# Performance work log

Measured on AMD Instinct MI355X. Metric: run time of the kernel, lower is better.

Reference implementation:

```python
import math
import jax, jax.numpy as jnp
import numpy as np

B, L, CIN, COUT = 128, 100, 55, 55
D, H, DFF, MODES = 512, 8, 512, 32
E = D // H
KERNELS = (12, 24)
NK = len(KERNELS)


def _pos_emb(length, d):
    pos = np.arange(length)[:, None].astype(np.float32)
    div = np.exp(np.arange(0, d, 2).astype(np.float32) * (-math.log(10000.0) / d))
    pe = np.zeros((length, d), dtype=np.float32)
    pe[:, 0::2] = np.sin(pos * div)
    pe[:, 1::2] = np.cos(pos * div)
    return jnp.asarray(pe)


def _circ_conv3(x, W):
    # Conv1d(kernel=3, padding=1, padding_mode='circular', bias=False); x:(B,L,C) W:(O,C,3)
    n = x.shape[1]
    xp = jnp.concatenate([x[:, -1:], x, x[:, :1]], axis=1)
    return (jnp.einsum('blc,oc->blo', xp[:, 0:n], W[:, :, 0]) +
            jnp.einsum('blc,oc->blo', xp[:, 1:n + 1], W[:, :, 1]) +
            jnp.einsum('blc,oc->blo', xp[:, 2:n + 2], W[:, :, 2]))


def _moving_avg(x, k):
    # replicate-pad then length-preserving mean filter (Autoformer moving_avg)
    front = jnp.repeat(x[:, :1], (k - 1) // 2, axis=1)
    end = jnp.repeat(x[:, -1:], k // 2, axis=1)
    xp = jnp.concatenate([front, x, end], axis=1)
    c = jnp.cumsum(xp, axis=1)
    c = jnp.concatenate([jnp.zeros_like(c[:, :1]), c], axis=1)
    return (c[:, k:] - c[:, :-k]) / float(k)


def _decomp(x, w, b):
    # series_decomp_multi with learned softmax mixing (Linear(1, NK))
    means = jnp.stack([_moving_avg(x, k) for k in KERNELS], axis=-1)  # (B,L,D,NK)
    mix = jax.nn.softmax(x[..., None] * w + b, axis=-1)
    mean = jnp.sum(means * mix, axis=-1)
    return x - mean, mean


def _my_layernorm(x, g, b):
    mu = x.mean(-1, keepdims=True)
    var = ((x - mu) ** 2).mean(-1, keepdims=True)
    xh = (x - mu) / jnp.sqrt(var + 1e-5) * g + b
    return xh - xh.mean(axis=1, keepdims=True)


def _fourier_block(q, Wc):
    # q:(B,L,H,E) -> rfft over L, per-mode complex GEMM with Wc:(H,E,E,MODES), irfft
    x = jnp.transpose(q, (0, 2, 3, 1))  # (B,H,E,L)
    xf = jnp.fft.rfft(x, axis=-1)
    sel = jnp.einsum('bhem,heom->bhom', xf[..., :MODES], Wc)
    nfreq = x.shape[-1] // 2 + 1
    out_ft = jnp.zeros(sel.shape[:-1] + (nfreq,), sel.dtype).at[..., :MODES].set(sel)
    out = jnp.fft.irfft(out_ft, n=x.shape[-1], axis=-1)
    return jnp.transpose(out, (0, 3, 1, 2))  # (B,L,H,E)


def _fourier_cross(q, k, Wc):
    # FourierCrossAttention: frequency-domain q*k attention with tanh activation, values = k
    xq = jnp.transpose(q, (0, 2, 3, 1))
    xk = jnp.transpose(k, (0, 2, 3, 1))
    qf = jnp.fft.rfft(xq, axis=-1)[..., :MODES]
    kf = jnp.fft.rfft(xk, axis=-1)[..., :MODES]
    qk = jnp.tanh(jnp.einsum('bhex,bhey->bhxy', qf, kf))
    qkv = jnp.einsum('bhxy,bhey->bhex', qk, kf)
    w = jnp.einsum('bhex,heox->bhox', qkv, Wc)
    nfreq = xq.shape[-1] // 2 + 1
    out_ft = jnp.zeros(w.shape[:-1] + (nfreq,), w.dtype).at[..., :MODES].set(w)
    out = jnp.fft.irfft(out_ft / float(D * D), n=xq.shape[-1], axis=-1)
    return jnp.transpose(out, (0, 3, 1, 2))


def _heads(x, W, b):
    y = x @ W.T + b
    return y.reshape(y.shape[0], y.shape[1], H, E)


def _gelu(x):
    return jax.nn.gelu(x, approximate=False)


def _forward(x, emb_enc_w, emb_dec_w, enc_proj_w, enc_proj_b, enc_sig_w, enc_sig_b,
             enc_four_wr, enc_four_wi, enc_ffn_w1, enc_ffn_w2, enc_dcmp_w, enc_dcmp_b,
             enc_norm_g, enc_norm_b, dec_proj_w, dec_proj_b, dec_four_wr, dec_four_wi,
             crs_proj_w, crs_proj_b, crs_four_wr, crs_four_wi, dec_ffn_w1, dec_ffn_w2,
             dec_dcmp_w, dec_dcmp_b, dec_trend_w, dec_norm_g, dec_norm_b,
             out_proj_w, out_proj_b):
    b, n, _ = x.shape
    dist = jnp.abs(jnp.arange(n)[:, None] - jnp.arange(n)[None, :]).astype(x.dtype)
    # seasonal-trend init decomposition
    trend_init = jnp.broadcast_to(x.mean(axis=1, keepdims=True), x.shape)
    seasonal_init = x - trend_init
    pe = _pos_emb(n, D)
    enc_four = enc_four_wr + 1j * enc_four_wi
    enc = _circ_conv3(x, emb_enc_w) + pe
    series_l, prior_l, sigma_l = [], [], []
    for i in range(enc_proj_w.shape[0]):  # e_layers (structurally distinct params)
        Wp, bp = enc_proj_w[i], enc_proj_b[i]
        q = _heads(enc, Wp[0], bp[0])
        k = _heads(enc, Wp[1], bp[1])
        v = _heads(enc, Wp[2], bp[2])  # projected but unused by FourierBlock (faithful)
        attn_out = _fourier_block(q, enc_four).reshape(b, n, D) @ Wp[3].T + bp[3]
        # Anomaly-Transformer association: series = softmax(QK^T/sqrt(E)), prior = Gaussian kernel
        scores = jnp.einsum('blhe,bshe->bhls', q, k) / math.sqrt(E)
        series = jax.nn.softmax(scores, axis=-1)
        sig = jnp.transpose(enc @ enc_sig_w[i].T + enc_sig_b[i], (0, 2, 1))  # (B,H,L)
        sig = jnp.power(3.0, jax.nn.sigmoid(5.0 * sig) + 1e-5) - 1.0
        prior = jnp.exp(-dist ** 2 / (2.0 * sig[..., None] ** 2)) / (math.sqrt(2.0 * math.pi) * sig[..., None])
        series_l.append(series); prior_l.append(prior); sigma_l.append(sig)
        h = enc + attn_out
        h, _ = _decomp(h, enc_dcmp_w[i, 0], enc_dcmp_b[i, 0])
        y = _gelu(h @ enc_ffn_w1[i].T) @ enc_ffn_w2[i].T
        enc, _ = _decomp(h + y, enc_dcmp_w[i, 1], enc_dcmp_b[i, 1])
    enc = _my_layernorm(enc, enc_norm_g, enc_norm_b)

    # decoder (d_layers = 1)
    dec = _circ_conv3(seasonal_init, emb_dec_w) + pe
    dec_four = dec_four_wr + 1j * dec_four_wi
    crs_four = crs_four_wr + 1j * crs_four_wi
    q = _heads(dec, dec_proj_w[0], dec_proj_b[0])
    sa = _fourier_block(q, dec_four).reshape(b, n, D) @ dec_proj_w[3].T + dec_proj_b[3]
    h = dec + sa
    h, t1 = _decomp(h, dec_dcmp_w[0], dec_dcmp_b[0])
    qc = _heads(h, crs_proj_w[0], crs_proj_b[0])
    kc = _heads(enc, crs_proj_w[1], crs_proj_b[1])
    ca = _fourier_cross(qc, kc, crs_four).reshape(b, n, D) @ crs_proj_w[3].T + crs_proj_b[3]
    h = h + ca
    h, t2 = _decomp(h, dec_dcmp_w[1], dec_dcmp_b[1])
    y = _gelu(h @ dec_ffn_w1.T) @ dec_ffn_w2.T
    h, t3 = _decomp(h + y, dec_dcmp_w[2], dec_dcmp_b[2])
    residual_trend = _circ_conv3(t1 + t2 + t3, dec_trend_w)  # (B,L,COUT)
    trend = trend_init + residual_trend
    h = _my_layernorm(h, dec_norm_g, dec_norm_b)
    seasonal = h @ out_proj_w.T + out_proj_b
    dec_out = trend + seasonal
    return dec_out, jnp.stack(series_l), jnp.stack(prior_l), jnp.stack(sigma_l)


def setup_inputs() -> dict:
    key = jax.random.key(0)
    ks = iter(jax.random.split(key, 64))

    def rn(shape, s=0.02):
        return s * jax.random.normal(next(ks), shape, dtype=jnp.float32)

    return dict(
        x=jax.random.normal(next(ks), (B, L, CIN), dtype=jnp.float32),
        emb_enc_w=rn((D, CIN, 3)), emb_dec_w=rn((D, CIN, 3)),
        enc_proj_w=rn((2, 4, D, D)), enc_proj_b=jnp.zeros((2, 4, D), jnp.float32),
        enc_sig_w=rn((2, H, D)), enc_sig_b=jnp.zeros((2, H), jnp.float32),
        enc_four_wr=rn((H, E, E, MODES)), enc_four_wi=rn((H, E, E, MODES)),
        enc_ffn_w1=rn((2, DFF, D)), enc_ffn_w2=rn((2, D, DFF)),
        enc_dcmp_w=rn((2, 2, NK), 1.0), enc_dcmp_b=jnp.zeros((2, 2, NK), jnp.float32),
        enc_norm_g=jnp.ones((D,), jnp.float32), enc_norm_b=jnp.zeros((D,), jnp.float32),
        dec_proj_w=rn((4, D, D)), dec_proj_b=jnp.zeros((4, D), jnp.float32),
        dec_four_wr=rn((H, E, E, MODES)), dec_four_wi=rn((H, E, E, MODES)),
        crs_proj_w=rn((4, D, D)), crs_proj_b=jnp.zeros((4, D), jnp.float32),
        crs_four_wr=rn((H, E, E, MODES)), crs_four_wi=rn((H, E, E, MODES)),
        dec_ffn_w1=rn((DFF, D)), dec_ffn_w2=rn((D, DFF)),
        dec_dcmp_w=rn((3, NK), 1.0), dec_dcmp_b=jnp.zeros((3, NK), jnp.float32),
        dec_trend_w=rn((COUT, D, 3)),
        dec_norm_g=jnp.ones((D,), jnp.float32), dec_norm_b=jnp.zeros((D,), jnp.float32),
        out_proj_w=rn((COUT, D)), out_proj_b=jnp.zeros((COUT,), jnp.float32),
    )


def reference(x, emb_enc_w, emb_dec_w, enc_proj_w, enc_proj_b, enc_sig_w, enc_sig_b,
              enc_four_wr, enc_four_wi, enc_ffn_w1, enc_ffn_w2, enc_dcmp_w, enc_dcmp_b,
              enc_norm_g, enc_norm_b, dec_proj_w, dec_proj_b, dec_four_wr, dec_four_wi,
              crs_proj_w, crs_proj_b, crs_four_wr, crs_four_wi, dec_ffn_w1, dec_ffn_w2,
              dec_dcmp_w, dec_dcmp_b, dec_trend_w, dec_norm_g, dec_norm_b,
              out_proj_w, out_proj_b):
    return _forward(x, emb_enc_w, emb_dec_w, enc_proj_w, enc_proj_b, enc_sig_w, enc_sig_b,
                    enc_four_wr, enc_four_wi, enc_ffn_w1, enc_ffn_w2, enc_dcmp_w, enc_dcmp_b,
                    enc_norm_g, enc_norm_b, dec_proj_w, dec_proj_b, dec_four_wr, dec_four_wi,
                    crs_proj_w, crs_proj_b, crs_four_wr, crs_four_wi, dec_ffn_w1, dec_ffn_w2,
                    dec_dcmp_w, dec_dcmp_b, dec_trend_w, dec_norm_g, dec_norm_b,
                    out_proj_w, out_proj_b)
```

## Files before the change

### kernel.cpp

```cpp
#include <hip/hip_runtime.h>
#include <hip/hip_bf16.h>
#include <cmath>

constexpr int B = 128, L = 100, CIN = 55, COUT = 55;
constexpr int D = 512, H = 8, DFF = 512, MODES = 32, E = 64;
constexpr int NK = 2;
constexpr int M_ROWS = B * L;
constexpr int KEMB = 192;
constexpr size_t BLD  = (size_t)B * L * D;
constexpr size_t BHEM = (size_t)B * H * E * MODES;
constexpr size_t BHLL = (size_t)B * H * L * L;
constexpr float INV_SQRT_2PI = 0.3989422804014327f;

static inline int cdiv(int a, int b) { return (a + b - 1) / b; }

typedef short shortx8 __attribute__((ext_vector_type(8)));
typedef float f32x4 __attribute__((ext_vector_type(4)));

__device__ inline unsigned short f2bf(float f)
{
    unsigned int u = __float_as_uint(f);
    unsigned int r = (u + 0x7FFFu + ((u >> 16) & 1u)) >> 16;
    return (unsigned short)r;
}
__device__ inline unsigned short f2bf_n(float f)
{
    union { __hip_bfloat16 h; unsigned short u; } cv;
    cv.h = __float2bfloat16(f);
    return cv.u;
}
__device__ inline float bf2f(unsigned short u)
{
    union { unsigned int i; float f; } c;
    c.i = (unsigned int)u << 16;
    return c.f;
}

__global__ void init_consts(float* __restrict__ pe)
{
    int idx = blockIdx.x * 256 + threadIdx.x;
    if (idx < L * D) {
        int l = idx / D, d = idx % D;
        int i2 = d & ~1;
        float div = expf((float)i2 * (-logf(10000.f) / (float)D));
        float ang = (float)l * div;
        pe[idx] = (d & 1) ? cosf(ang) : sinf(ang);
    }
}

__global__ void init_tw(unsigned short* __restrict__ twf, unsigned short* __restrict__ twi)
{
    int idx = blockIdx.x * 256 + threadIdx.x;
    if (idx >= 64 * 128) return;
    {
        int mp = idx / 128, t = idx % 128;
        float v = 0.f;
        if (t < L) {
            if (mp < 32) v = cosf(2.f * 3.14159265358979323846f * (float)mp * (float)t / (float)L);
            else v = -sinf(2.f * 3.14159265358979323846f * (float)(mp - 32) * (float)t / (float)L);
        }
        twf[idx] = f2bf(v);
    }
    {
        int t = idx / 64, mp = idx % 64;
        float v = 0.f;
        if (t < L) {
            if (mp == 0) v = 1.f;
            else if (mp < 32) v = 2.f * cosf(2.f * 3.14159265358979323846f * (float)mp * (float)t / (float)L);
            else if (mp == 32) v = 0.f;
            else v = -2.f * sinf(2.f * 3.14159265358979323846f * (float)(mp - 32) * (float)t / (float)L);
        }
        twi[idx] = f2bf(v);
    }
}

__global__ void xmean_kernel(const float* __restrict__ x, float* __restrict__ xm)
{
    int idx = blockIdx.x * 256 + threadIdx.x;
    if (idx >= B * CIN) return;
    int b = idx / CIN, c = idx % CIN;
    float s = 0.f;
    for (int l = 0; l < L; ++l) s += x[((size_t)b * L + l) * CIN + c];
    xm[idx] = s * (1.f / (float)L);
}

struct PrepArgs {
    const float* src[7];
    unsigned short* dst[7];
    int n4[7];
    const float* emb_enc; const float* emb_dec; const float* trend_w; const float* seas_w;
    unsigned short* d_embenc; unsigned short* d_embdec; unsigned short* d_trd; unsigned short* d_seas;
};
__global__ __launch_bounds__(256) void prep_all(PrepArgs a, int total4, int padTotal)
{
    for (int i = blockIdx.x * 256 + threadIdx.x; i < total4 + padTotal; i += gridDim.x * 256) {
        if (i < total4) {
            int idx = i, s = 0;
            while (idx >= a.n4[s]) { idx -= a.n4[s]; ++s; }
            float4 v = *(const float4*)&a.src[s][(size_t)idx * 4];
            ushort4 h;
            h.x = f2bf(v.x); h.y = f2bf(v.y); h.z = f2bf(v.z); h.w = f2bf(v.w);
            *(ushort4*)&a.dst[s][(size_t)idx * 4] = h;
            continue;
        }
        int p = i - total4;
        if (p < D * KEMB) {
            int r = p / KEMB, k = p % KEMB;
            a.d_embenc[p] = (k < CIN * 3) ? f2bf(a.emb_enc[(size_t)r * (CIN * 3) + k]) : (unsigned short)0;
        } else if ((p -= D * KEMB) < D * KEMB) {
            int r = p / KEMB, k = p % KEMB;
            a.d_embdec[p] = (k < CIN * 3) ? f2bf(a.emb_dec[(size_t)r * (CIN * 3) + k]) : (unsigned short)0;
        } else if ((p -= D * KEMB) < 192 * D) {
            int n = p / D, d = p % D;
            int j = n / 64, o = n % 64;
            a.d_trd[p] = (o < COUT) ? f2bf(a.trend_w[(size_t)o * (D * 3) + d * 3 + j]) : (unsigned short)0;
        } else {
            p -= 192 * D;
            int r = p / D, k = p % D;
            a.d_seas[p] = (r < COUT) ? f2bf(a.seas_w[(size_t)r * D + k]) : (unsigned short)0;
        }
    }
}

__global__ __launch_bounds__(256) void transpose_w(const float* __restrict__ wr, const float* __restrict__ wi,
                                                   float2* __restrict__ wt)
{
    int h = blockIdx.x / E, e = blockIdx.x % E;
    __shared__ float tr[64][33], ti[64][33];
    for (int i = threadIdx.x; i < E * MODES; i += 256) {
        int o = i / MODES, m = i % MODES;
        size_t s = (((size_t)h * E + e) * E + o) * MODES + m;
        tr[o][m] = wr[s]; ti[o][m] = wi[s];
    }
    __syncthreads();
    for (int i = threadIdx.x; i < MODES * E; i += 256) {
        int m = i / E, o = i % E;
        wt[(((size_t)h * MODES + m) * E + e) * E + o] = make_float2(tr[o][m], ti[o][m]);
    }
}

__global__ void im2col_emb(const float* __restrict__ x, const float* __restrict__ xmean,
                           unsigned short* __restrict__ A2)
{
    int idx = blockIdx.x * 256 + threadIdx.x;
    if (idx >= M_ROWS * KEMB) return;
    int k = idx % KEMB, m = idx / KEMB;
    float v = 0.f;
    if (k < CIN * 3) {
        int c = k / 3, j = k % 3;
        int l = m % L, b = m / L;
        int ls = l + j - 1; ls = (ls + L) % L;
        v = x[((size_t)b * L + ls) * CIN + c];
        if (xmean) v -= xmean[(size_t)b * CIN + c];
    }
    A2[idx] = f2bf(v);
}

template<int BN>
__global__ __launch_bounds__(256) void gemm_mfma(const unsigned short* __restrict__ A,
                                                 const unsigned short* __restrict__ Wb,
                                                 const float* __restrict__ bias, const float* __restrict__ pe,
                                                 float* __restrict__ C, unsigned short* __restrict__ Cb,
                                                 int Nout, int K, int act, int accum)
{
    constexpr int NI = BN / 32;
    constexpr int BI = BN / 64;
    __shared__ unsigned short As[2][128][40];
    __shared__ unsigned short Bs[2][BN][40];
    int tid = threadIdx.x;
    int row0 = blockIdx.y * 128, col0 = blockIdx.x * BN;
    int wid = tid >> 6, lane = tid & 63;
    int wm = wid >> 1, wn = wid & 1;
    int lrow = lane & 15, kg = lane >> 4;
    int ar = tid >> 2, ac8 = (tid & 3) * 8;
    f32x4 acc[4][NI] = {};
    shortx8 rah[2], rbh[BI];

    auto loadG = [&](int k0) {
#pragma unroll
        for (int p = 0; p < 2; ++p)
            rah[p] = *(const shortx8*)&A[(size_t)(row0 + p * 64 + ar) * K + k0 + ac8];
#pragma unroll
        for (int p = 0; p < BI; ++p)
            rbh[p] = *(const shortx8*)&Wb[(size_t)(col0 + p * 64 + ar) * K + k0 + ac8];
    };
    auto storeLDS = [&](int buf) {
#pragma unroll
        for (int p = 0; p < 2; ++p)
            *(shortx8*)&As[buf][p * 64 + ar][ac8] = rah[p];
#pragma unroll
        for (int p = 0; p < BI; ++p)
            *(shortx8*)&Bs[buf][p * 64 + ar][ac8] = rbh[p];
    };

    int nk = K >> 5;
    loadG(0);
    storeLDS(0);
    if (nk > 1) loadG(32);
    __syncthreads();
    int cur = 0;
    for (int s = 0; s < nk; ++s) {
        if (s + 1 < nk) {
            storeLDS(cur ^ 1);
            if (s + 2 < nk) loadG((s + 2) << 5);
        }
        shortx8 av[4], bv[NI];
#pragma unroll
        for (int mi = 0; mi < 4; ++mi)
            av[mi] = *(const shortx8*)&As[cur][wm * 64 + mi * 16 + lrow][kg * 8];
#pragma unroll
        for (int ni = 0; ni < NI; ++ni)
            bv[ni] = *(const shortx8*)&Bs[cur][wn * (BN / 2) + ni * 16 + lrow][kg * 8];
#pragma unroll
        for (int mi = 0; mi < 4; ++mi)
#pragma unroll
            for (int ni = 0; ni < NI; ++ni)
                acc[mi][ni] = __builtin_amdgcn_mfma_f32_16x16x32_bf16(av[mi], bv[ni], acc[mi][ni], 0, 0, 0);
        if (s + 1 < nk) __syncthreads();
        cur ^= 1;
    }
#pragma unroll
    for (int mi = 0; mi < 4; ++mi) {
#pragma unroll
        for (int ni = 0; ni < NI; ++ni) {
            int col = col0 + wn * (BN / 2) + ni * 16 + lrow;
            if (col >= Nout) continue;
#pragma unroll
            for (int r = 0; r < 4; ++r) {
                int row = row0 + wm * 64 + mi * 16 + kg * 4 + r;
                float v = acc[mi][ni][r];
                if (bias) v += bias[col];
                if (pe) v += pe[(size_t)(row % L) * Nout + col];
                if (act) v = 0.5f * v * (1.f + erff(v * 0.70710678118654752f));
                size_t o = (size_t)row * Nout + col;
                if (Cb) Cb[o] = f2bf_n(v);
                else if (accum) C[o] += v;
                else C[o] = v;
            }
        }
    }
}

__global__ __launch_bounds__(256) void scores_softmax(const unsigned short* __restrict__ QK,
                                                      float* __restrict__ out)
{
    int bh = blockIdx.x, b = bh / H, h = bh % H;
    int pass = blockIdx.y;
    __shared__ unsigned short Ks[112][72];
    __shared__ unsigned short Qs[64][72];
    int tid = threadIdx.x;
    int srow = tid >> 4, sc4 = (tid & 15) * 4;
#pragma unroll
    for (int i = 0; i < 7; ++i) {
        int r = i * 16 + srow;
        ushort4 hh = {0, 0, 0, 0};
        if (r < L) hh = *(const ushort4*)&QK[((size_t)b * L + r) * 1024 + 512 + h * E + sc4];
        *(ushort4*)&Ks[r][sc4] = hh;
    }
#pragma unroll
    for (int i = 0; i < 4; ++i) {
        int r = i * 16 + srow;
        int gr = pass * 64 + r;
        ushort4 hh = {0, 0, 0, 0};
        if (gr < L) hh = *(const ushort4*)&QK[((size_t)b * L + gr) * 1024 + h * E + sc4];
        *(ushort4*)&Qs[r][sc4] = hh;
    }
    __syncthreads();
    int wid = tid >> 6, lane = tid & 63;
    int lrow = lane & 15, kg = lane >> 4;
    f32x4 acc[7] = {};
#pragma unroll
    for (int ks = 0; ks < 2; ++ks) {
        shortx8 aq = *(const shortx8*)&Qs[wid * 16 + lrow][ks * 32 + kg * 8];
#pragma unroll
        for (int tj = 0; tj < 7; ++tj) {
            shortx8 bk = *(const shortx8*)&Ks[tj * 16 + lrow][ks * 32 + kg * 8];
            acc[tj] = __builtin_amdgcn_mfma_f32_16x16x32_bf16(aq, bk, acc[tj], 0, 0, 0);
        }
    }
    float mx[4] = {-1e30f, -1e30f, -1e30f, -1e30f};
#pragma unroll
    for (int tj = 0; tj < 7; ++tj) {
        bool valid = (tj * 16 + lrow) < L;
#pragma unroll
        for (int r = 0; r < 4; ++r) {
            float v = acc[tj][r] * 0.125f;
            acc[tj][r] = valid ? v : -1e30f;
            if (valid) mx[r] = fmaxf(mx[r], v);
        }
    }
#pragma unroll
    for (int off = 1; off < 16; off <<= 1)
#pragma unroll
        for (int r = 0; r < 4; ++r) mx[r] = fmaxf(mx[r], __shfl_xor(mx[r], off));
    float sum[4] = {0.f, 0.f, 0.f, 0.f};
#pragma unroll
    for (int tj = 0; tj < 7; ++tj)
#pragma unroll
        for (int r = 0; r < 4; ++r) {
            float e = expf(acc[tj][r] - mx[r]);
            acc[tj][r] = e;
            sum[r] += e;
        }
#pragma unroll
    for (int off = 1; off < 16; off <<= 1)
#pragma unroll
        for (int r = 0; r < 4; ++r) sum[r] += __shfl_xor(sum[r], off);
    float inv[4];
#pragma unroll
    for (int r = 0; r < 4; ++r) inv[r] = 1.f / sum[r];
    float* base = out + (size_t)bh * L * L;
#pragma unroll
    for (int r = 0; r < 4; ++r) {
        int row = pass * 64 + wid * 16 + kg * 4 + r;
        if (row >= L) continue;
#pragma unroll
        for (int tj = 0; tj < 7; ++tj) {
            int col = tj * 16 + lrow;
            if (col < L) base[(size_t)row * L + col] = acc[tj][r] * inv[r];
        }
    }
}

__global__ void trend_combine(const float* __restrict__ Y, const float* __restrict__ xmean,
                              float* __restrict__ dec_out)
{
    int idx = blockIdx.x * 256 + threadIdx.x;
    if (idx >= B * L * COUT) return;
    int o = idx % COUT; int l = (idx / COUT) % L; int b = idx / (COUT * L);
    int lm = (l + L - 1) % L, lp = (l + 1) % L;
    float v = xmean[(size_t)b * CIN + o]
            + Y[((size_t)b * L + lm) * 192 + o]
            + Y[((size_t)b * L + l ) * 192 + 64 + o]
            + Y[((size_t)b * L + lp) * 192 + 128 + o];
    dec_out[idx] = v;
}

__global__ __launch_bounds__(256) void dft_mfma(const unsigned short* __restrict__ X,
                                                const unsigned short* __restrict__ twf,
                                                float2* __restrict__ xf, int stride)
{
    int b = blockIdx.x / H, h = blockIdx.x % H;
    __shared__ unsigned short Xs[64][136];
    int tid = threadIdx.x;
    for (int i = tid; i < L * E / 4; i += 256) {
        int t = i >> 4, e4 = (i & 15) * 4;
        ushort4 u = *(const ushort4*)&X[((size_t)b * L + t) * stride + h * E + e4];
        Xs[e4][t] = u.x; Xs[e4 + 1][t] = u.y; Xs[e4 + 2][t] = u.z; Xs[e4 + 3][t] = u.w;
    }
    for (int i = tid; i < 64 * 28; i += 256) {
        int e = i / 28, t = L + i % 28;
        Xs[e][t] = 0;
    }
    __syncthreads();
    int wid = tid >> 6, lane = tid & 63;
    int lrow = lane & 15, kg = lane >> 4;
    f32x4 acc[4] = {};
#pragma unroll
    for (int k0 = 0; k0 < 4; ++k0) {
        shortx8 bx = *(const shortx8*)&Xs[wid * 16 + lrow][k0 * 32 + kg * 8];
#pragma unroll
        for (int mi = 0; mi < 4; ++mi) {
            shortx8 aw = *(const shortx8*)&twf[(size_t)(mi * 16 + lrow) * 128 + k0 * 32 + kg * 8];
            acc[mi] = __builtin_amdgcn_mfma_f32_16x16x32_bf16(aw, bx, acc[mi], 0, 0, 0);
        }
    }
    int e = wid * 16 + lrow;
#pragma unroll
    for (int mi = 0; mi < 2; ++mi)
#pragma unroll
        for (int r = 0; r < 4; ++r) {
            int m = mi * 16 + kg * 4 + r;
            xf[((size_t)(h * MODES + m) * B + b) * E + e] = make_float2(acc[mi][r], acc[mi + 2][r]);
        }
}

__global__ __launch_bounds__(256) void idft_mfma(const float2* __restrict__ sel,
                                                 const unsigned short* __restrict__ twi,
                                                 unsigned short* __restrict__ out, float scale)
{
    int b = blockIdx.x / H, h = blockIdx.x % H;
    __shared__ unsigned short Ss[64][72];
    int tid = threadIdx.x;
    for (int i = tid; i < MODES * E; i += 256) {
        int m = i >> 6, o = i & 63;
        float2 v = sel[((size_t)(h * MODES + m) * B + b) * E + o];
        Ss[o][m] = f2bf_n(v.x);
        Ss[o][m + 32] = f2bf_n(v.y);
    }
    __syncthreads();
    int wid = tid >> 6, lane = tid & 63;
    int lrow = lane & 15, kg = lane >> 4;
    f32x4 acc[2][4] = {};
#pragma unroll
    for (int k0 = 0; k0 < 2; ++k0) {
        shortx8 bs[4];
#pragma unroll
        for (int ni = 0; ni < 4; ++ni)
            bs[ni] = *(const shortx8*)&Ss[ni * 16 + lrow][k0 * 32 + kg * 8];
#pragma unroll
        for (int ti = 0; ti < 2; ++ti) {
            shortx8 at = *(const shortx8*)&twi[(size_t)((wid * 2 + ti) * 16 + lrow) * 64 + k0 * 32 + kg * 8];
#pragma unroll
            for (int ni = 0; ni < 4; ++ni)
                acc[ti][ni] = __builtin_amdgcn_mfma_f32_16x16x32_bf16(at, bs[ni], acc[ti][ni], 0, 0, 0);
        }
    }
#pragma unroll
    for (int ti = 0; ti < 2; ++ti)
#pragma unroll
        for (int ni = 0; ni < 4; ++ni)
#pragma unroll
            for (int r = 0; r < 4; ++r) {
                int t = (wid * 2 + ti) * 16 + kg * 4 + r;
                if (t < L) {
                    int o = ni * 16 + lrow;
                    out[((size_t)b * L + t) * D + h * E + o] = f2bf_n(acc[ti][ni][r] * scale);
                }
            }
}

__global__ __launch_bounds__(256) void mode_gemm2(float2* __restrict__ xf, const float2* __restrict__ wt)
{
    int hm = blockIdx.x;
    int bt = blockIdx.y;
    __shared__ float2 Wc[E][E];
    __shared__ float2 Ac[32][E];
    for (int i = threadIdx.x; i < E * E; i += 256) Wc[i / E][i % E] = wt[(size_t)hm * (E * E) + i];
    for (int i = threadIdx.x; i < 32 * E; i += 256)
        Ac[i / E][i % E] = xf[((size_t)hm * B + bt * 32 + i / E) * E + i % E];
    __syncthreads();
    int o = threadIdx.x & 63, bb = threadIdx.x >> 6;
    float2 acc[8];
#pragma unroll
    for (int j = 0; j < 8; ++j) acc[j] = make_float2(0.f, 0.f);
    for (int e = 0; e < E; ++e) {
        float2 w = Wc[e][o];
#pragma unroll
        for (int j = 0; j < 8; ++j) {
            float2 a = Ac[bb * 8 + j][e];
            acc[j].x += a.x * w.x - a.y * w.y;
            acc[j].y += a.x * w.y + a.y * w.x;
        }
    }
#pragma unroll
    for (int j = 0; j < 8; ++j)
        xf[((size_t)hm * B + bt * 32 + bb * 8 + j) * E + o] = acc[j];
}

__global__ __launch_bounds__(256) void fourier_qk(const float2* __restrict__ qf, float2* __restrict__ kf)
{
    int b = blockIdx.x / H, h = blockIdx.x % H;
    __shared__ float2 qm[MODES][E + 1], km[MODES][E + 1], vm[MODES][E + 1];
    __shared__ float tr[MODES][MODES + 1], ti[MODES][MODES + 1];
    for (int i = threadIdx.x; i < MODES * E; i += 256) {
        int m = i / E, e = i % E;
        size_t idx = ((size_t)(h * MODES + m) * B + b) * E + e;
        qm[m][e] = qf[idx];
        km[m][e] = kf[idx];
    }
    __syncthreads();
    for (int i = threadIdx.x; i < MODES * MODES; i += 256) {
        int x = i / MODES, y = i % MODES;
        float re = 0.f, im = 0.f;
        for (int e = 0; e < E; ++e) {
            float2 a = qm[x][e], k2 = km[y][e];
            re += a.x * k2.x - a.y * k2.y;
            im += a.x * k2.y + a.y * k2.x;
        }
        float aa = fminf(fmaxf(2.f * re, -30.f), 30.f);
        float b2 = 2.f * im;
        float den = coshf(aa) + cosf(b2);
        tr[x][y] = sinhf(aa) / den;
        ti[x][y] = sinf(b2) / den;
    }
    __syncthreads();
    for (int i = threadIdx.x; i < MODES * E; i += 256) {
        int x = i / E, e = i % E;
        float re = 0.f, im = 0.f;
        for (int y = 0; y < MODES; ++y) {
            float ar = tr[x][y], ai = ti[x][y];
            float2 kk = km[y][e];
            re += ar * kk.x - ai * kk.y;
            im += ar * kk.y + ai * kk.x;
        }
        vm[x][e] = make_float2(re, im);
    }
    __syncthreads();
    for (int i = threadIdx.x; i < MODES * E; i += 256) {
        int m = i / E, e = i % E;
        kf[((size_t)(h * MODES + m) * B + b) * E + e] = vm[m][e];
    }
}

__global__ __launch_bounds__(256) void sigma_prior(const unsigned short* __restrict__ enc,
                                                   const float* __restrict__ w,
                                                   const float* __restrict__ bias,
                                                   float* __restrict__ sig_out, float* __restrict__ prior)
{
    __shared__ float wsh[H][D];
    for (int i = threadIdx.x; i < H * D; i += 256) wsh[i / D][i % D] = w[i];
    __syncthreads();
    int wid = threadIdx.x / 64, lane = threadIdx.x % 64;
    int row = blockIdx.x * 4 + wid;
    const unsigned short* p = enc + (size_t)row * D;
    float xv[8];
#pragma unroll
    for (int i = 0; i < 8; ++i) xv[i] = bf2f(p[lane + i * 64]);
    int b = row / L, l = row % L;
#pragma unroll
    for (int h = 0; h < H; ++h) {
        float s = 0.f;
#pragma unroll
        for (int i = 0; i < 8; ++i) s += xv[i] * wsh[h][lane + i * 64];
        for (int off = 32; off; off >>= 1) s += __shfl_xor(s, off);
        float acc = s + bias[h];
        float sg = 1.f / (1.f + expf(-5.f * acc));
        float val = expf((sg + 1e-5f) * 1.0986122886681098f) - 1.f;
        if (lane == 0) sig_out[((size_t)b * H + h) * L + l] = val;
        float inv2 = 1.f / (2.f * val * val);
        float coef = INV_SQRT_2PI / val;
        float* pr = prior + (((size_t)b * H + h) * L + l) * L;
        for (int sc = lane; sc < L; sc += 64) {
            float d = (float)abs(l - sc);
            pr[sc] = expf(-d * d * inv2) * coef;
        }
    }
}

__global__ __launch_bounds__(256) void decomp_kernel(const unsigned short* __restrict__ in1,
                                                     const unsigned short* __restrict__ in2,
                                                     const float* __restrict__ w, const float* __restrict__ bc,
                                                     unsigned short* __restrict__ res, float* __restrict__ trend,
                                                     unsigned short* __restrict__ trend16, int tmode)
{
    int b = blockIdx.x / (D / 64);
    int d0 = (blockIdx.x % (D / 64)) * 64;
    __shared__ float P[125][65];
    __shared__ float qtot[4][64];
    int tid = threadIdx.x;
    int dd = tid & 63, q = tid >> 6;
    int p0 = q * 31;
    float run = 0.f;
#pragma unroll
    for (int i = 0; i < 31; ++i) {
        int p = p0 + i;
        int j = min(max(p - 12, 0), L - 1);
        size_t g = ((size_t)b * L + j) * D + d0 + dd;
        float v = bf2f(in1[g]);
        if (in2) v += bf2f(in2[g]);
        run += v;
        P[p + 1][dd] = run;
    }
    qtot[q][dd] = run;
    if (tid < 64) P[0][dd] = 0.f;
    __syncthreads();
    if (q > 0) {
        float off = qtot[0][dd];
        if (q > 1) off += qtot[1][dd];
        if (q > 2) off += qtot[2][dd];
#pragma unroll
        for (int i = 0; i < 31; ++i)
            P[p0 + i + 1][dd] += off;
    }
    __syncthreads();
    float w0 = w[0], w1 = w[1], b0 = bc[0], b1 = bc[1];
    for (int i = tid; i < L * 64; i += 256) {
        int l = i >> 6, d2 = i & 63;
        float s12 = P[l + 19][d2] - P[l + 7][d2];
        float s24 = P[l + 25][d2] - P[l + 1][d2];
        float x = P[l + 13][d2] - P[l + 12][d2];
        float m0 = s12 * (1.f / 12.f), m1 = s24 * (1.f / 24.f);
        float z0 = x * w0 + b0, z1 = x * w1 + b1;
        float zm = fmaxf(z0, z1);
        float e0 = expf(z0 - zm), e1 = expf(z1 - zm);
        float p0f = e0 / (e0 + e1);
        float mean = m0 * p0f + m1 * (1.f - p0f);
        size_t g = ((size_t)b * L + l) * D + d0 + d2;
        res[g] = f2bf_n(x - mean);
        if (tmode == 1) trend[g] = mean;
        else if (tmode == 2) {
            float tv = trend[g] + mean;
            trend[g] = tv;
            if (trend16) trend16[g] = f2bf_n(tv);
        }
    }
}

__global__ __launch_bounds__(256) void ln_colsub(const unsigned short* __restrict__ x,
                                                 const float* __restrict__ g, const float* __restrict__ bb,
                                                 unsigned short* __restrict__ out)
{
    int b = blockIdx.x;
    __shared__ unsigned short xs[L][D];
    __shared__ float colmean[D];
    __shared__ float gs[D], bs2[D];
    int tid = threadIdx.x;
    for (int i = tid; i < L * D / 8; i += 256) {
        int l = i / 64, c8 = (i % 64) * 8;
        *(shortx8*)&xs[l][c8] = *(const shortx8*)&x[((size_t)b * L + l) * D + c8];
    }
    for (int i = tid; i < D; i += 256) { gs[i] = g[i]; bs2[i] = bb[i]; }
    __syncthreads();
    int wid = tid >> 6, lane = tid & 63;
    for (int l = wid; l < L; l += 4) {
        float v[8];
        float s = 0.f, s2 = 0.f;
#pragma unroll
        for (int i = 0; i < 8; ++i) {
            v[i] = bf2f(xs[l][lane + i * 64]);
            s += v[i]; s2 += v[i] * v[i];
        }
        for (int off = 32; off; off >>= 1) { s += __shfl_xor(s, off); s2 += __shfl_xor(s2, off); }
        float mu = s / (float)D;
        float var = s2 / (float)D - mu * mu;
        float rstd = rsqrtf(var + 1e-5f);
#pragma unroll
        for (int i = 0; i < 8; ++i) {
            int d = lane + i * 64;
            xs[l][d] = f2bf_n((v[i] - mu) * rstd * gs[d] + bs2[d]);
        }
    }
    __syncthreads();
    for (int c = tid; c < D; c += 256) {
        float s = 0.f;
        for (int l = 0; l < L; ++l) s += bf2f(xs[l][c]);
        colmean[c] = s * (1.f / (float)L);
    }
    __syncthreads();
    for (int i = tid; i < L * D; i += 256) {
        int l = i / D, c = i % D;
        out[((size_t)b * L + l) * D + c] = f2bf_n(bf2f(xs[l][c]) - colmean[c]);
    }
}

extern "C" void kernel_launch(void* const* d_in, const int* in_sizes, int n_in,
                              void* d_out, int out_size, void* d_ws, size_t ws_size,
                              hipStream_t stream)
{
    const float* x           = (const float*)d_in[0];
    const float* emb_enc_w   = (const float*)d_in[1];
    const float* emb_dec_w   = (const float*)d_in[2];
    const float* enc_proj_w  = (const float*)d_in[3];
    const float* enc_proj_b  = (const float*)d_in[4];
    const float* enc_sig_w   = (const float*)d_in[5];
    const float* enc_sig_b   = (const float*)d_in[6];
    const float* enc_four_wr = (const float*)d_in[7];
    const float* enc_four_wi = (const float*)d_in[8];
    const float* enc_ffn_w1  = (const float*)d_in[9];
    const float* enc_ffn_w2  = (const float*)d_in[10];
    const float* enc_dcmp_w  = (const float*)d_in[11];
    const float* enc_dcmp_b  = (const float*)d_in[12];
    const float* enc_norm_g  = (const float*)d_in[13];
    const float* enc_norm_b  = (const float*)d_in[14];
    const float* dec_proj_w  = (const float*)d_in[15];
    const float* dec_proj_b  = (const float*)d_in[16];
    const float* dec_four_wr = (const float*)d_in[17];
    const float* dec_four_wi = (const float*)d_in[18];
    const float* crs_proj_w  = (const float*)d_in[19];
    const float* crs_proj_b  = (const float*)d_in[20];
    const float* crs_four_wr = (const float*)d_in[21];
    const float* crs_four_wi = (const float*)d_in[22];
    const float* dec_ffn_w1  = (const float*)d_in[23];
    const float* dec_ffn_w2  = (const float*)d_in[24];
    const float* dec_dcmp_w  = (const float*)d_in[25];
    const float* dec_dcmp_b  = (const float*)d_in[26];
    const float* dec_trend_w = (const float*)d_in[27];
    const float* dec_norm_g  = (const float*)d_in[28];
    const float* dec_norm_b  = (const float*)d_in[29];
    const float* out_proj_w  = (const float*)d_in[30];
    const float* out_proj_b  = (const float*)d_in[31];

    float* ws = (float*)d_ws;
    size_t off = 0;
    float* pe    = ws + off; off += (size_t)L * D;
    float* xmean = ws + off; off += (size_t)B * CIN;
    float* bufF  = ws + off; off += BLD;
    float* tacc  = ws + off; off += BLD;
    float2* xfc  = (float2*)(ws + off); off += 2 * BHEM;
    float2* kfc  = (float2*)(ws + off); off += 2 * BHEM;
    float2* wtb  = (float2*)(ws + off); off += 2 * (size_t)H * MODES * E * E;
    unsigned short* qk16 = (unsigned short*)(ws + off); off += BLD;
    unsigned short* e16  = (unsigned short*)(ws + off); off += BLD / 2;
    unsigned short* c16  = (unsigned short*)(ws + off); off += BLD / 2;
    unsigned short* d16  = (unsigned short*)(ws + off); off += BLD / 2;
    unsigned short* h16  = (unsigned short*)(ws + off); off += BLD / 2;
    unsigned short* t16  = (unsigned short*)(ws + off); off += BLD / 2;
    unsigned short* im16 = (unsigned short*)(ws + off); off += (size_t)M_ROWS * KEMB / 2;
    unsigned short* wbf_encproj = (unsigned short*)(ws + off); off += (size_t)2 * 4 * D * D / 2;
    unsigned short* wbf_ffn1    = (unsigned short*)(ws + off); off += (size_t)2 * DFF * D / 2;
    unsigned short* wbf_ffn2    = (unsigned short*)(ws + off); off += (size_t)2 * D * DFF / 2;
    unsigned short* wbf_decproj = (unsigned short*)(ws + off); off += (size_t)4 * D * D / 2;
    unsigned short* wbf_crsproj = (unsigned short*)(ws + off); off += (size_t)4 * D * D / 2;
    unsigned short* wbf_dffn1   = (unsigned short*)(ws + off); off += (size_t)DFF * D / 2;
    unsigned short* wbf_dffn2   = (unsigned short*)(ws + off); off += (size_t)D * DFF / 2;
    unsigned short* wbf_embenc  = (unsigned short*)(ws + off); off += (size_t)D * KEMB / 2;
    unsigned short* wbf_embdec  = (unsigned short*)(ws + off); off += (size_t)D * KEMB / 2;
    unsigned short* wbf_trd     = (unsigned short*)(ws + off); off += (size_t)192 * D / 2;
    unsigned short* wbf_seas    = (unsigned short*)(ws + off); off += (size_t)64 * D / 2;
    unsigned short* twf         = (unsigned short*)(ws + off); off += (size_t)64 * 128 / 2;
    unsigned short* twi         = (unsigned short*)(ws + off); off += (size_t)128 * 64 / 2;
    unsigned short* a16 = qk16;
    unsigned short* b16 = qk16 + BLD;

    float* out       = (float*)d_out;
    float* dec_out   = out;
    float* series_out= out + (size_t)B * L * COUT;
    float* prior_out = series_out + 2 * BHLL;
    float* sigma_out = prior_out + 2 * BHLL;

    const int BH = B * H;

    init_consts<<<200, 256, 0, stream>>>(pe);
    init_tw<<<32, 256, 0, stream>>>(twf, twi);
    xmean_kernel<<<cdiv(B * CIN, 256), 256, 0, stream>>>(x, xmean);

    PrepArgs pa;
    pa.src[0] = enc_proj_w; pa.dst[0] = wbf_encproj; pa.n4[0] = 2 * 4 * D * D / 4;
    pa.src[1] = enc_ffn_w1; pa.dst[1] = wbf_ffn1;    pa.n4[1] = 2 * DFF * D / 4;
    pa.src[2] = enc_ffn_w2; pa.dst[2] = wbf_ffn2;    pa.n4[2] = 2 * D * DFF / 4;
    pa.src[3] = dec_proj_w; pa.dst[3] = wbf_decproj; pa.n4[3] = 4 * D * D / 4;
    pa.src[4] = crs_proj_w; pa.dst[4] = wbf_crsproj; pa.n4[4] = 4 * D * D / 4;
    pa.src[5] = dec_ffn_w1; pa.dst[5] = wbf_dffn1;   pa.n4[5] = DFF * D / 4;
    pa.src[6] = dec_ffn_w2; pa.dst[6] = wbf_dffn2;   pa.n4[6] = D * DFF / 4;
    pa.emb_enc = emb_enc_w; pa.emb_dec = emb_dec_w; pa.trend_w = dec_trend_w; pa.seas_w = out_proj_w;
    pa.d_embenc = wbf_embenc; pa.d_embdec = wbf_embdec; pa.d_trd = wbf_trd; pa.d_seas = wbf_seas;
    int total4 = 0;
    for (int s = 0; s < 7; ++s) total4 += pa.n4[s];
    int padTotal = 2 * D * KEMB + 192 * D + 64 * D;
    prep_all<<<2048, 256, 0, stream>>>(pa, total4, padTotal);
    transpose_w<<<H * E, 256, 0, stream>>>(enc_four_wr, enc_four_wi, wtb);

    auto gemm = [&](const unsigned short* A, const unsigned short* Wb, const float* bias, const float* pe_,
                    float* C, unsigned short* Cb, int N, int Nout, int K, int act, int accum) {
        if (N % 128 == 0) {
            dim3 grid(N / 128, M_ROWS / 128);
            gemm_mfma<128><<<grid, 256, 0, stream>>>(A, Wb, bias, pe_, C, Cb, Nout, K, act, accum);
        } else {
            dim3 grid(N / 64, M_ROWS / 128);
            gemm_mfma<64><<<grid, 256, 0, stream>>>(A, Wb, bias, pe_, C, Cb, Nout, K, act, accum);
        }
    };
    dim3 mg_grid(H * MODES, B / 32);
    dim3 sc_grid(BH, 2);

    im2col_emb<<<cdiv(M_ROWS * KEMB, 256), 256, 0, stream>>>(x, nullptr, im16);
    gemm(im16, wbf_embenc, nullptr, pe, nullptr, e16, D, D, KEMB, 0, 0);

    for (int i = 0; i < 2; ++i) {
        const unsigned short* Wp = wbf_encproj + (size_t)i * 4 * D * D;
        const float* bp = enc_proj_b + (size_t)i * 4 * D;
        float* series_i = series_out + (size_t)i * BHLL;
        float* prior_i  = prior_out  + (size_t)i * BHLL;
        float* sigma_i  = sigma_out  + (size_t)i * B * H * L;

        gemm(e16, Wp, bp, nullptr, nullptr, qk16, 1024, 1024, D, 0, 0);
        dft_mfma<<<BH, 256, 0, stream>>>(qk16, twf, xfc, 1024);
        mode_gemm2<<<mg_grid, 256, 0, stream>>>(xfc, wtb);
        idft_mfma<<<BH, 256, 0, stream>>>(xfc, twi, c16, 1.f / (float)L);
        gemm(c16, Wp + (size_t)3 * D * D, bp + 3 * D, nullptr, nullptr, d16, D, D, D, 0, 0);
        scores_softmax<<<sc_grid, 256, 0, stream>>>(qk16, series_i);
        sigma_prior<<<M_ROWS / 4, 256, 0, stream>>>(e16, enc_sig_w + (size_t)i * H * D,
                                                    enc_sig_b + (size_t)i * H, sigma_i, prior_i);
        decomp_kernel<<<B * (D / 64), 256, 0, stream>>>(e16, d16, enc_dcmp_w + (size_t)(i * 2 + 0) * NK,
                                                        enc_dcmp_b + (size_t)(i * 2 + 0) * NK, h16, nullptr, nullptr, 0);
        gemm(h16, wbf_ffn1 + (size_t)i * DFF * D, nullptr, nullptr, nullptr, c16, DFF, DFF, D, 1, 0);
        gemm(c16, wbf_ffn2 + (size_t)i * D * DFF, nullptr, nullptr, nullptr, d16, D, D, DFF, 0, 0);
        decomp_kernel<<<B * (D / 64), 256, 0, stream>>>(h16, d16, enc_dcmp_w + (size_t)(i * 2 + 1) * NK,
                                                        enc_dcmp_b + (size_t)(i * 2 + 1) * NK, e16, nullptr, nullptr, 0);
    }
    ln_colsub<<<B, 256, 0, stream>>>(e16, enc_norm_g, enc_norm_b, e16);

    transpose_w<<<H * E, 256, 0, stream>>>(dec_four_wr, dec_four_wi, wtb);
    im2col_emb<<<cdiv(M_ROWS * KEMB, 256), 256, 0, stream>>>(x, xmean, im16);
    gemm(im16, wbf_embdec, nullptr, pe, nullptr, a16, D, D, KEMB, 0, 0);
    gemm(a16, wbf_decproj, dec_proj_b, nullptr, nullptr, b16, D, D, D, 0, 0);
    dft_mfma<<<BH, 256, 0, stream>>>(b16, twf, xfc, D);
    mode_gemm2<<<mg_grid, 256, 0, stream>>>(xfc, wtb);
    idft_mfma<<<BH, 256, 0, stream>>>(xfc, twi, c16, 1.f / (float)L);
    gemm(c16, wbf_decproj + (size_t)3 * D * D, dec_proj_b + 3 * D, nullptr, nullptr, d16, D, D, D, 0, 0);
    decomp_kernel<<<B * (D / 64), 256, 0, stream>>>(a16, d16, dec_dcmp_w, dec_dcmp_b, h16, tacc, nullptr, 1);

    gemm(h16, wbf_crsproj, crs_proj_b, nullptr, nullptr, b16, D, D, D, 0, 0);
    dft_mfma<<<BH, 256, 0, stream>>>(b16, twf, xfc, D);
    gemm(e16, wbf_crsproj + (size_t)D * D, crs_proj_b + D, nullptr, nullptr, b16, D, D, D, 0, 0);
    dft_mfma<<<BH, 256, 0, stream>>>(b16, twf, kfc, D);
    transpose_w<<<H * E, 256, 0, stream>>>(crs_four_wr, crs_four_wi, wtb);
    fourier_qk<<<BH, 256, 0, stream>>>(xfc, kfc);
    mode_gemm2<<<mg_grid, 256, 0, stream>>>(kfc, wtb);
    idft_mfma<<<BH, 256, 0, stream>>>(kfc, twi, c16, 1.f / ((float)L * (float)D * (float)D));
    gemm(c16, wbf_crsproj + (size_t)3 * D * D, crs_proj_b + 3 * D, nullptr, nullptr, d16, D, D, D, 0, 0);
    decomp_kernel<<<B * (D / 64), 256, 0, stream>>>(h16, d16, dec_dcmp_w + NK, dec_dcmp_b + NK, a16, tacc, nullptr, 2);

    gemm(a16, wbf_dffn1, nullptr, nullptr, nullptr, c16, DFF, DFF, D, 1, 0);
    gemm(c16, wbf_dffn2, nullptr, nullptr, nullptr, d16, D, D, DFF, 0, 0);
    decomp_kernel<<<B * (D / 64), 256, 0, stream>>>(a16, d16, dec_dcmp_w + 2 * NK, dec_dcmp_b + 2 * NK, b16, tacc, t16, 2);

    gemm(t16, wbf_trd, nullptr, nullptr, bufF, nullptr, 192, 192, D, 0, 0);
    trend_combine<<<cdiv(B * L * COUT, 256), 256, 0, stream>>>(bufF, xmean, dec_out);

    ln_colsub<<<B, 256, 0, stream>>>(b16, dec_norm_g, dec_norm_b, d16);
    gemm(d16, wbf_seas, out_proj_b, nullptr, dec_out, nullptr, 64, COUT, D, 0, 1);
}
```

Baseline: 1.284 ms.

## Run per-mode complex Fourier GEMM on bf16 MFMA with pre-split weights

The per-mode complex GEMM in the Fourier blocks was scalar fp32 FMA work on float2. It now runs on bf16 MFMA instructions. The weight transpose kernel writes real and imaginary parts as separate bf16 planes in an N-by-K layout, and the new kernel converts activations to bf16 in shared memory. The complex product is formed from four real MFMA products. This removes scalar ALU cost and halves the weight bytes, at the price of bf16 rounding on the activations and weights of the frequency-domain product.

```diff
diff --git a/kernel.cpp b/kernel.cpp
--- a/kernel.cpp
+++ b/kernel.cpp
@@ -122,20 +122,22 @@
     }
 }
 
-__global__ __launch_bounds__(256) void transpose_w(const float* __restrict__ wr, const float* __restrict__ wi,
-                                                   float2* __restrict__ wt)
-{
-    int h = blockIdx.x / E, e = blockIdx.x % E;
+__global__ __launch_bounds__(256) void transpose_wb(const float* __restrict__ wr, const float* __restrict__ wi,
+                                                    unsigned short* __restrict__ wt)
+{
+    int h = blockIdx.x / E, o = blockIdx.x % E;
     __shared__ float tr[64][33], ti[64][33];
     for (int i = threadIdx.x; i < E * MODES; i += 256) {
-        int o = i / MODES, m = i % MODES;
+        int e = i >> 5, m = i & 31;
         size_t s = (((size_t)h * E + e) * E + o) * MODES + m;
-        tr[o][m] = wr[s]; ti[o][m] = wi[s];
+        tr[e][m] = wr[s]; ti[e][m] = wi[s];
     }
     __syncthreads();
     for (int i = threadIdx.x; i < MODES * E; i += 256) {
-        int m = i / E, o = i % E;
-        wt[(((size_t)h * MODES + m) * E + e) * E + o] = make_float2(tr[o][m], ti[o][m]);
+        int m = i >> 6, e = i & 63;
+        size_t base = ((size_t)(h * MODES + m) * 2) * 4096 + (size_t)o * 64 + e;
+        wt[base] = f2bf(tr[e][m]);
+        wt[base + 4096] = f2bf(ti[e][m]);
     }
 }
 
@@ -420,32 +422,56 @@
             }
 }
 
-__global__ __launch_bounds__(256) void mode_gemm2(float2* __restrict__ xf, const float2* __restrict__ wt)
+__global__ __launch_bounds__(256) void mode_gemm_mfma(float2* __restrict__ xf,
+                                                      const unsigned short* __restrict__ wt)
 {
     int hm = blockIdx.x;
     int bt = blockIdx.y;
-    __shared__ float2 Wc[E][E];
-    __shared__ float2 Ac[32][E];
-    for (int i = threadIdx.x; i < E * E; i += 256) Wc[i / E][i % E] = wt[(size_t)hm * (E * E) + i];
-    for (int i = threadIdx.x; i < 32 * E; i += 256)
-        Ac[i / E][i % E] = xf[((size_t)hm * B + bt * 32 + i / E) * E + i % E];
-    __syncthreads();
-    int o = threadIdx.x & 63, bb = threadIdx.x >> 6;
-    float2 acc[8];
-#pragma unroll
-    for (int j = 0; j < 8; ++j) acc[j] = make_float2(0.f, 0.f);
-    for (int e = 0; e < E; ++e) {
-        float2 w = Wc[e][o];
-#pragma unroll
-        for (int j = 0; j < 8; ++j) {
-            float2 a = Ac[bb * 8 + j][e];
-            acc[j].x += a.x * w.x - a.y * w.y;
-            acc[j].y += a.x * w.y + a.y * w.x;
-        }
-    }
-#pragma unroll
-    for (int j = 0; j < 8; ++j)
-        xf[((size_t)hm * B + bt * 32 + bb * 8 + j) * E + o] = acc[j];
+    __shared__ unsigned short XrS[32][72], XiS[32][72];
+    __shared__ unsigned short WrS[64][72], WiS[64][72];
+    int tid = threadIdx.x;
+    for (int i = tid; i < 32 * 64; i += 256) {
+        int row = i >> 6, e = i & 63;
+        float2 v = xf[((size_t)hm * B + bt * 32 + row) * E + e];
+        XrS[row][e] = f2bf_n(v.x);
+        XiS[row][e] = f2bf_n(v.y);
+    }
+    const unsigned short* wr = wt + (size_t)hm * 2 * 4096;
+    const unsigned short* wi = wr + 4096;
+    for (int i = tid; i < 512; i += 256) {
+        int o = i >> 3, e8 = (i & 7) * 8;
+        *(shortx8*)&WrS[o][e8] = *(const shortx8*)&wr[(size_t)o * 64 + e8];
+        *(shortx8*)&WiS[o][e8] = *(const shortx8*)&wi[(size_t)o * 64 + e8];
+    }
+    __syncthreads();
+    int wid = tid >> 6, lane = tid & 63;
+    int lrow = lane & 15, kg = lane >> 4;
+    int n0 = wid * 16;
+    f32x4 p1[2] = {}, p2[2] = {}, p3[2] = {}, p4[2] = {};
+#pragma unroll
+    for (int ks = 0; ks < 2; ++ks) {
+        shortx8 bR = *(const shortx8*)&WrS[n0 + lrow][ks * 32 + kg * 8];
+        shortx8 bI = *(const shortx8*)&WiS[n0 + lrow][ks * 32 + kg * 8];
+#pragma unroll
+        for (int m = 0; m < 2; ++m) {
+            shortx8 aR = *(const shortx8*)&XrS[m * 16 + lrow][ks * 32 + kg * 8];
+            shortx8 aI = *(const shortx8*)&XiS[m * 16 + lrow][ks * 32 + kg * 8];
+            p1[m] = __builtin_amdgcn_mfma_f32_16x16x32_bf16(aR, bR, p1[m], 0, 0, 0);
+            p2[m] = __builtin_amdgcn_mfma_f32_16x16x32_bf16(aI, bI, p2[m], 0, 0, 0);
+            p3[m] = __builtin_amdgcn_mfma_f32_16x16x32_bf16(aR, bI, p3[m], 0, 0, 0);
+            p4[m] = __builtin_amdgcn_mfma_f32_16x16x32_bf16(aI, bR, p4[m], 0, 0, 0);
+        }
+    }
+    __syncthreads();
+#pragma unroll
+    for (int m = 0; m < 2; ++m)
+#pragma unroll
+        for (int r = 0; r < 4; ++r) {
+            int row = m * 16 + kg * 4 + r;
+            int o = n0 + lrow;
+            xf[((size_t)hm * B + bt * 32 + row) * E + o] =
+                make_float2(p1[m][r] - p2[m][r], p3[m][r] + p4[m][r]);
+        }
 }
 
 __global__ __launch_bounds__(256) void fourier_qk(const float2* __restrict__ qf, float2* __restrict__ kf)
@@ -679,7 +705,7 @@
     float* tacc  = ws + off; off += BLD;
     float2* xfc  = (float2*)(ws + off); off += 2 * BHEM;
     float2* kfc  = (float2*)(ws + off); off += 2 * BHEM;
-    float2* wtb  = (float2*)(ws + off); off += 2 * (size_t)H * MODES * E * E;
+    unsigned short* wtbf = (unsigned short*)(ws + off); off += (size_t)H * MODES * 2 * E * E / 2;
     unsigned short* qk16 = (unsigned short*)(ws + off); off += BLD;
     unsigned short* e16  = (unsigned short*)(ws + off); off += BLD / 2;
     unsigned short* c16  = (unsigned short*)(ws + off); off += BLD / 2;
@@ -729,7 +755,7 @@
     for (int s = 0; s < 7; ++s) total4 += pa.n4[s];
     int padTotal = 2 * D * KEMB + 192 * D + 64 * D;
     prep_all<<<2048, 256, 0, stream>>>(pa, total4, padTotal);
-    transpose_w<<<H * E, 256, 0, stream>>>(enc_four_wr, enc_four_wi, wtb);
+    transpose_wb<<<H * E, 256, 0, stream>>>(enc_four_wr, enc_four_wi, wtbf);
 
     auto gemm = [&](const unsigned short* A, const unsigned short* Wb, const float* bias, const float* pe_,
                     float* C, unsigned short* Cb, int N, int Nout, int K, int act, int accum) {
@@ -756,7 +782,7 @@
 
         gemm(e16, Wp, bp, nullptr, nullptr, qk16, 1024, 1024, D, 0, 0);
         dft_mfma<<<BH, 256, 0, stream>>>(qk16, twf, xfc, 1024);
-        mode_gemm2<<<mg_grid, 256, 0, stream>>>(xfc, wtb);
+        mode_gemm_mfma<<<mg_grid, 256, 0, stream>>>(xfc, wtbf);
         idft_mfma<<<BH, 256, 0, stream>>>(xfc, twi, c16, 1.f / (float)L);
         gemm(c16, Wp + (size_t)3 * D * D, bp + 3 * D, nullptr, nullptr, d16, D, D, D, 0, 0);
         scores_softmax<<<sc_grid, 256, 0, stream>>>(qk16, series_i);
@@ -771,12 +797,12 @@
     }
     ln_colsub<<<B, 256, 0, stream>>>(e16, enc_norm_g, enc_norm_b, e16);
 
-    transpose_w<<<H * E, 256, 0, stream>>>(dec_four_wr, dec_four_wi, wtb);
+    transpose_wb<<<H * E, 256, 0, stream>>>(dec_four_wr, dec_four_wi, wtbf);
     im2col_emb<<<cdiv(M_ROWS * KEMB, 256), 256, 0, stream>>>(x, xmean, im16);
     gemm(im16, wbf_embdec, nullptr, pe, nullptr, a16, D, D, KEMB, 0, 0);
     gemm(a16, wbf_decproj, dec_proj_b, nullptr, nullptr, b16, D, D, D, 0, 0);
     dft_mfma<<<BH, 256, 0, stream>>>(b16, twf, xfc, D);
-    mode_gemm2<<<mg_grid, 256, 0, stream>>>(xfc, wtb);
+    mode_gemm_mfma<<<mg_grid, 256, 0, stream>>>(xfc, wtbf);
     idft_mfma<<<BH, 256, 0, stream>>>(xfc, twi, c16, 1.f / (float)L);
     gemm(c16, wbf_decproj + (size_t)3 * D * D, dec_proj_b + 3 * D, nullptr, nullptr, d16, D, D, D, 0, 0);
     decomp_kernel<<<B * (D / 64), 256, 0, stream>>>(a16, d16, dec_dcmp_w, dec_dcmp_b, h16, tacc, nullptr, 1);
@@ -785,9 +811,9 @@
     dft_mfma<<<BH, 256, 0, stream>>>(b16, twf, xfc, D);
     gemm(e16, wbf_crsproj + (size_t)D * D, crs_proj_b + D, nullptr, nullptr, b16, D, D, D, 0, 0);
     dft_mfma<<<BH, 256, 0, stream>>>(b16, twf, kfc, D);
-    transpose_w<<<H * E, 256, 0, stream>>>(crs_four_wr, crs_four_wi, wtb);
+    transpose_wb<<<H * E, 256, 0, stream>>>(crs_four_wr, crs_four_wi, wtbf);
     fourier_qk<<<BH, 256, 0, stream>>>(xfc, kfc);
-    mode_gemm2<<<mg_grid, 256, 0, stream>>>(kfc, wtb);
+    mode_gemm_mfma<<<mg_grid, 256, 0, stream>>>(kfc, wtbf);
     idft_mfma<<<BH, 256, 0, stream>>>(kfc, twi, c16, 1.f / ((float)L * (float)D * (float)D));
     gemm(c16, wbf_crsproj + (size_t)3 * D * D, crs_proj_b + 3 * D, nullptr, nullptr, d16, D, D, D, 0, 0);
     decomp_kernel<<<B * (D / 64), 256, 0, stream>>>(h16, d16, dec_dcmp_w + NK, dec_dcmp_b + NK, a16, tacc, nullptr, 2);
```

Result: faster. 1.185 ms (-7.7%).
